# Kernel optimization log

Hardware: AMD Instinct MI355X
Metric: run time of the kernel (lower is better)

## Reference

```python
import jax, jax.numpy as jnp
import numpy as np

B, H, W, DIM = 8, 64, 64, 768
NH = 12
HD = DIM // NH            # 64
WS = 14                   # window size
N = WS * WS               # 196 tokens per window
MLP = 4 * DIM             # 3072
EPS = 1e-5


def layernorm(x, w, b):
    mu = jnp.mean(x, axis=-1, keepdims=True)
    var = jnp.var(x, axis=-1, keepdims=True)
    return (x - mu) * jax.lax.rsqrt(var + EPS) * w + b


def window_partition(x, ws):
    b, h, w, c = x.shape
    pad_h = (ws - h % ws) % ws
    pad_w = (ws - w % ws) % ws
    x = jnp.pad(x, ((0, 0), (0, pad_h), (0, pad_w), (0, 0)))
    hp, wp = h + pad_h, w + pad_w
    x = x.reshape(b, hp // ws, ws, wp // ws, ws, c)
    windows = x.transpose(0, 1, 3, 2, 4, 5).reshape(-1, ws, ws, c)
    return windows, (hp, wp)


def window_unpartition(windows, ws, pad_hw, hw):
    hp, wp = pad_hw
    h, w = hw
    b = windows.shape[0] // (hp * wp // ws // ws)
    x = windows.reshape(b, hp // ws, wp // ws, ws, ws, -1)
    x = x.transpose(0, 1, 3, 2, 4, 5).reshape(b, hp, wp, -1)
    return x[:, :h, :w, :]


def setup_inputs() -> dict:
    key = jax.random.key(0)
    ks = jax.random.split(key, 8)
    f = lambda k, shape: jax.random.normal(k, shape, jnp.float32) * 0.02
    return {
        "x": jax.random.normal(ks[0], (B, H, W, DIM), jnp.float32),
        "n1_w": jnp.ones((DIM,), jnp.float32),
        "n1_b": jnp.zeros((DIM,), jnp.float32),
        "qkv_w": f(ks[1], (DIM, 3 * DIM)),
        "qkv_b": jnp.zeros((3 * DIM,), jnp.float32),
        "proj_w": f(ks[2], (DIM, DIM)),
        "proj_b": jnp.zeros((DIM,), jnp.float32),
        "rel_pos_h": f(ks[3], (2 * WS - 1, HD)),
        "rel_pos_w": f(ks[4], (2 * WS - 1, HD)),
        "n2_w": jnp.ones((DIM,), jnp.float32),
        "n2_b": jnp.zeros((DIM,), jnp.float32),
        "lin1_w": f(ks[5], (DIM, MLP)),
        "lin1_b": jnp.zeros((MLP,), jnp.float32),
        "lin2_w": f(ks[6], (MLP, DIM)),
        "lin2_b": jnp.zeros((DIM,), jnp.float32),
    }


def reference(x, n1_w, n1_b, qkv_w, qkv_b, proj_w, proj_b, rel_pos_h, rel_pos_w,
              n2_w, n2_b, lin1_w, lin1_b, lin2_w, lin2_b):
    shortcut = x
    h = layernorm(x, n1_w, n1_b)
    win, pad_hw = window_partition(h, WS)           # [Bw, WS, WS, DIM]
    bw = win.shape[0]
    qkv = win.reshape(bw, N, DIM) @ qkv_w + qkv_b   # [Bw, N, 3*DIM]
    qkv = qkv.reshape(bw, N, 3, NH, HD).transpose(2, 0, 3, 1, 4)
    qkv = qkv.reshape(3, bw * NH, N, HD)
    q, k, v = qkv[0], qkv[1], qkv[2]
    scale = HD ** -0.5
    attn = jnp.einsum('bqc,bkc->bqk', q * scale, k)  # [Bw*NH, N, N]
    # decomposed rel-pos bias; q_size == k_size == WS so no interpolation
    coords = jnp.arange(WS)[:, None] - jnp.arange(WS)[None, :] + (WS - 1)
    Rh = rel_pos_h[coords]                           # [WS, WS, HD]
    Rw = rel_pos_w[coords]
    r_q = q.reshape(-1, WS, WS, HD)
    rel_h = jnp.einsum('bhwc,hkc->bhwk', r_q, Rh)
    rel_w = jnp.einsum('bhwc,wkc->bhwk', r_q, Rw)
    attn = (attn.reshape(-1, WS, WS, WS, WS)
            + rel_h[:, :, :, :, None]
            + rel_w[:, :, :, None, :]).reshape(-1, N, N)
    attn = jax.nn.softmax(attn, axis=-1)
    out = jnp.einsum('bqk,bkc->bqc', attn, v)        # [Bw*NH, N, HD]
    out = out.reshape(bw, NH, WS, WS, HD).transpose(0, 2, 3, 1, 4)
    out = out.reshape(bw, WS, WS, DIM) @ proj_w + proj_b
    out = window_unpartition(out, WS, pad_hw, (H, W))
    x = shortcut + out
    h2 = layernorm(x, n2_w, n2_b)
    mlp = jax.nn.gelu(h2 @ lin1_w + lin1_b, approximate=False) @ lin2_w + lin2_b
    return x + mlp
```

## Files before the change

### kernel.cpp

```cpp
#include <hip/hip_runtime.h>
#include <hip/hip_bf16.h>
#include <stdint.h>

typedef __attribute__((ext_vector_type(8))) short bf16x8;
typedef __attribute__((ext_vector_type(4))) float f32x4;

__device__ __forceinline__ float bf2f(unsigned short u){
  union { unsigned int i; float f; } v; v.i = ((unsigned int)u) << 16; return v.f;
}
__device__ __forceinline__ unsigned short f2bf(float f){
  union { float f; unsigned int i; } v; v.f = f;
  return (unsigned short)((v.i + 0x7FFFu + ((v.i >> 16) & 1u)) >> 16);
}

__device__ __forceinline__ void gload16(const void* g, void* l){
  __builtin_amdgcn_global_load_lds(
      (const __attribute__((address_space(1))) void*)g,
      (__attribute__((address_space(3))) void*)l, 16, 0, 0);
}

#define VT_OFF 0L
#define Q_OFF  30720000L
#define K_OFF  60825600L

__global__ __launch_bounds__(256) void k_castT(const float* __restrict__ W,
                                               unsigned short* __restrict__ Wt,
                                               int K, int N){
  __shared__ float tl[32][33];
  int ntn = N >> 5;
  int kt = blockIdx.x / ntn, nt = blockIdx.x % ntn;
  int r = threadIdx.x >> 5, c = threadIdx.x & 31;
#pragma unroll
  for (int rr = 0; rr < 4; rr++){
    int row = (kt << 5) + r + (rr << 3);
    tl[r + (rr << 3)][c] = W[(long)row * N + (nt << 5) + c];
  }
  __syncthreads();
#pragma unroll
  for (int rr = 0; rr < 4; rr++){
    int n = (nt << 5) + r + (rr << 3);
    int k = (kt << 5) + c;
    Wt[(long)n * K + k] = f2bf(tl[c][r + (rr << 3)]);
  }
}

__global__ __launch_bounds__(256) void k_ln(const float* __restrict__ X,
                                            const float* __restrict__ w,
                                            const float* __restrict__ b,
                                            unsigned short* __restrict__ out,
                                            int mode){
  int p = blockIdx.x, t = threadIdx.x;
  unsigned short* orow = out + (long)p * 768;
  const float* xrow;
  if (mode == 1){
    int win = p / 196, tok = p - win * 196;
    int bb = win / 25, wrem = win - bb * 25;
    int wy = wrem / 5, wx = wrem - wy * 5;
    int ty = tok / 14, tx = tok - ty * 14;
    int yy = wy * 14 + ty, xx = wx * 14 + tx;
    if (yy >= 64 || xx >= 64){
      for (int j = t; j < 768; j += 256) orow[j] = 0;
      return;
    }
    xrow = X + (long)((bb * 64 + yy) * 64 + xx) * 768;
  } else {
    xrow = X + (long)p * 768;
  }
  float v0 = xrow[t], v1 = xrow[t + 256], v2 = xrow[t + 512];
  float s = v0 + v1 + v2, q = v0 * v0 + v1 * v1 + v2 * v2;
#pragma unroll
  for (int off = 32; off; off >>= 1){ s += __shfl_down(s, off); q += __shfl_down(q, off); }
  __shared__ float ps[4], pq[4], mv[2];
  int wid = t >> 6;
  if ((t & 63) == 0){ ps[wid] = s; pq[wid] = q; }
  __syncthreads();
  if (t == 0){
    float S = ps[0] + ps[1] + ps[2] + ps[3];
    float Q = pq[0] + pq[1] + pq[2] + pq[3];
    float mu = S * (1.0f / 768.0f);
    float var = Q * (1.0f / 768.0f) - mu * mu;
    mv[0] = mu; mv[1] = rsqrtf(var + 1e-5f);
  }
  __syncthreads();
  float mu = mv[0], rs = mv[1];
  orow[t]       = f2bf((v0 - mu) * rs * w[t]       + b[t]);
  orow[t + 256] = f2bf((v1 - mu) * rs * w[t + 256] + b[t + 256]);
  orow[t + 512] = f2bf((v2 - mu) * rs * w[t + 512] + b[t + 512]);
}

template<int MODE>
__global__ __launch_bounds__(256) void k_gemm(const unsigned short* __restrict__ A,
                                              const unsigned short* __restrict__ Bt,
                                              const float* bias,
                                              unsigned short* obf,
                                              float* of32,
                                              const float* addsrc,
                                              int M, int N, int K, int lda, int ldb,
                                              int tilesN){
  __shared__ __align__(16) unsigned short lA[2 * 128 * 32];
  __shared__ __align__(16) unsigned short lB[2 * 128 * 32];
  int t = threadIdx.x;

  int nwg = gridDim.x, bid = blockIdx.x;
  int qq = nwg >> 3, rr = nwg & 7;
  int xcd = bid & 7, oo = bid >> 3;
  int wg = (xcd < rr ? xcd * (qq + 1) : rr * (qq + 1) + (xcd - rr) * qq) + oo;
  int tm = wg / tilesN, tn = wg % tilesN;

  int sl = (t & 3) ^ ((t >> 3) & 3);
  const unsigned short* ga[2]; const unsigned short* gb[2];
#pragma unroll
  for (int c2 = 0; c2 < 2; c2++){
    int i = tm * 128 + c2 * 64 + (t >> 2); if (i > M - 1) i = M - 1;
    ga[c2] = A + (long)i * lda + sl * 8;
    int n = tn * 128 + c2 * 64 + (t >> 2);
    gb[c2] = Bt + (long)n * ldb + sl * 8;
  }

  int lm = t & 15, lg = (t & 63) >> 4, wv = t >> 6;
  int wr = wv >> 1, wc = wv & 1;
  int laneoff = lm * 32 + ((lg ^ ((lm >> 1) & 3)) * 8);

  f32x4 acc[4][4];
#pragma unroll
  for (int a1 = 0; a1 < 4; a1++)
#pragma unroll
    for (int b1 = 0; b1 < 4; b1++) acc[a1][b1] = (f32x4){0.f, 0.f, 0.f, 0.f};

  const int nt = K >> 5;
  {
    unsigned short* la = lA + t * 8;
    unsigned short* lb = lB + t * 8;
    gload16(ga[0], la);
    gload16(ga[1], la + 2048);
    gload16(gb[0], lb);
    gload16(gb[1], lb + 2048);
  }

  for (int tt = 0; tt < nt; tt++){
    int cur = tt & 1;
    if (tt + 1 < nt){
      int k0 = (tt + 1) << 5;
      unsigned short* la = lA + (cur ^ 1) * 4096 + t * 8;
      unsigned short* lb = lB + (cur ^ 1) * 4096 + t * 8;
      gload16(ga[0] + k0, la);
      gload16(ga[1] + k0, la + 2048);
      gload16(gb[0] + k0, lb);
      gload16(gb[1] + k0, lb + 2048);
      asm volatile("s_waitcnt vmcnt(4)" ::: "memory");
    } else {
      asm volatile("s_waitcnt vmcnt(0)" ::: "memory");
    }
    __builtin_amdgcn_sched_barrier(0);
    __builtin_amdgcn_s_barrier();
    __builtin_amdgcn_sched_barrier(0);

    const unsigned short* lap = lA + cur * 4096;
    const unsigned short* lbp = lB + cur * 4096;
    bf16x8 af[4], bfr[4];
#pragma unroll
    for (int mi = 0; mi < 4; mi++)
      af[mi] = *(const bf16x8*)(lap + (wr * 64 + mi * 16) * 32 + laneoff);
#pragma unroll
    for (int ni = 0; ni < 4; ni++)
      bfr[ni] = *(const bf16x8*)(lbp + (wc * 64 + ni * 16) * 32 + laneoff);
    __builtin_amdgcn_s_setprio(1);
#pragma unroll
    for (int mi = 0; mi < 4; mi++)
#pragma unroll
      for (int ni = 0; ni < 4; ni++)
        acc[mi][ni] = __builtin_amdgcn_mfma_f32_16x16x32_bf16(af[mi], bfr[ni], acc[mi][ni], 0, 0, 0);
    __builtin_amdgcn_s_setprio(0);
    __builtin_amdgcn_sched_barrier(0);
    __builtin_amdgcn_s_barrier();
  }

  int i0 = tm * 128 + wr * 64, j0 = tn * 128 + wc * 64;
#pragma unroll
  for (int mi = 0; mi < 4; mi++){
#pragma unroll
    for (int ni = 0; ni < 4; ni++){
      int jc = j0 + ni * 16 + lm;
      float bv = bias ? bias[jc] : 0.0f;
#pragma unroll
      for (int r = 0; r < 4; r++){
        int ir = i0 + mi * 16 + lg * 4 + r;
        float v = acc[mi][ni][r] + bv;
        if (MODE == 0){
          if (ir < M){
            int which = jc / 768, jj = jc - which * 768;
            int head = jj >> 6, cc = jj & 63;
            int win = ir / 196, tok = ir - win * 196;
            long wh = win * 12 + head;
            if (which == 0)      obf[Q_OFF + (wh * 196 + tok) * 64 + cc] = f2bf(v);
            else if (which == 1) obf[K_OFF + (wh * 196 + tok) * 64 + cc] = f2bf(v);
            else                 obf[VT_OFF + (wh * 64 + cc) * 200 + tok] = f2bf(v);
          }
        } else if (MODE == 1){
          if (ir < M){
            int win = ir / 196, tok = ir - win * 196;
            int bb = win / 25, wrem = win - bb * 25;
            int wy = wrem / 5, wx = wrem - wy * 5;
            int yy = wy * 14 + tok / 14, xx = wx * 14 + tok % 14;
            if (yy < 64 && xx < 64){
              long row = (long)((bb * 64 + yy) * 64 + xx);
              of32[row * 768 + jc] = v + addsrc[row * 768 + jc];
            }
          }
        } else if (MODE == 2){
          float g = 0.5f * v * (1.0f + erff(v * 0.70710678118654752f));
          obf[(long)ir * N + jc] = f2bf(g);
        } else {
          long idx = (long)ir * N + jc;
          of32[idx] = v + addsrc[idx];
        }
      }
    }
  }
}

#define KSW(r,c)  ((r) * 64 + ((c) ^ (((r) & 7) << 3)))
#define PSW(q,k)  ((q) * 32 + ((k) ^ (((q) & 3) << 3)))
#define DYN_ATTN  53760
__global__ __launch_bounds__(256, 2) void k_attn(const unsigned short* __restrict__ qb,
                                                 const unsigned short* __restrict__ kb,
                                                 const unsigned short* __restrict__ vtb,
                                                 const float* __restrict__ rph,
                                                 const float* __restrict__ rpw,
                                                 unsigned short* __restrict__ out){
  extern __shared__ __align__(16) char dynsm[];
  unsigned short* Ks = (unsigned short*)dynsm;
  unsigned short* Vt = (unsigned short*)(dynsm + 25088);
  __shared__ __align__(16) unsigned short Pscr[4][2][16 * 32];
  __shared__ unsigned short relhb[2744], relwb[2744];

  int t = threadIdx.x;
  int wh = blockIdx.x;
  int win = wh / 12, head = wh - win * 12;
  const unsigned short* qg  = qb  + (long)wh * 196 * 64;
  const unsigned short* kg  = kb  + (long)wh * 196 * 64;
  const unsigned short* vtg = vtb + (long)wh * 64 * 200;

  int lane = t & 63, wv = t >> 6;
  int lm = lane & 15, lg = lane >> 4;

  for (int ch = t; ch < 1568; ch += 256){
    int row = ch >> 3, c16 = ch & 7;
    gload16(kg + row * 64 + ((c16 ^ (row & 7)) << 3), (char*)Ks + ch * 16);
  }
  {
    int4 zero4 = {0, 0, 0, 0};
    for (int ch = t; ch < 1792; ch += 256){
      int row = ch / 28, c16 = ch - row * 28;
      if (c16 < 25) gload16(vtg + row * 200 + c16 * 8, (char*)Vt + ch * 16);
      else          *(int4*)((char*)Vt + ch * 16) = zero4;
    }
  }

  for (int ty = wv; ty < 14; ty += 4){
    {
      int qa = ty * 14 + lm; if (qa > 195) qa = 195;
      bf16x8 a0 = *(const bf16x8*)(&qg[qa * 64 + lg * 8]);
      bf16x8 a1 = *(const bf16x8*)(&qg[qa * 64 + 32 + lg * 8]);
      int ri = ty - lm + 13; ri = ri < 0 ? 0 : (ri > 26 ? 26 : ri);
      const float* bp = rph + ri * 64 + lg * 8;
      float4 c0 = *(const float4*)(bp),      c1 = *(const float4*)(bp + 4);
      float4 c2 = *(const float4*)(bp + 32), c3 = *(const float4*)(bp + 36);
      bf16x8 b0 = {(short)f2bf(c0.x),(short)f2bf(c0.y),(short)f2bf(c0.z),(short)f2bf(c0.w),
                   (short)f2bf(c1.x),(short)f2bf(c1.y),(short)f2bf(c1.z),(short)f2bf(c1.w)};
      bf16x8 b1 = {(short)f2bf(c2.x),(short)f2bf(c2.y),(short)f2bf(c2.z),(short)f2bf(c2.w),
                   (short)f2bf(c3.x),(short)f2bf(c3.y),(short)f2bf(c3.z),(short)f2bf(c3.w)};
      f32x4 d = (f32x4){0.f, 0.f, 0.f, 0.f};
      d = __builtin_amdgcn_mfma_f32_16x16x32_bf16(a0, b0, d, 0, 0, 0);
      d = __builtin_amdgcn_mfma_f32_16x16x32_bf16(a1, b1, d, 0, 0, 0);
#pragma unroll
      for (int r = 0; r < 4; r++){
        int txr = lg * 4 + r;
        if (txr < 14 && lm < 14) relhb[(ty * 14 + txr) * 14 + lm] = f2bf(d[r]);
      }
    }
    {
      int qa = lm * 14 + ty; if (qa > 195) qa = 195;
      bf16x8 a0 = *(const bf16x8*)(&qg[qa * 64 + lg * 8]);
      bf16x8 a1 = *(const bf16x8*)(&qg[qa * 64 + 32 + lg * 8]);
      int ri = ty - lm + 13; ri = ri < 0 ? 0 : (ri > 26 ? 26 : ri);
      const float* bp = rpw + ri * 64 + lg * 8;
      float4 c0 = *(const float4*)(bp),      c1 = *(const float4*)(bp + 4);
      float4 c2 = *(const float4*)(bp + 32), c3 = *(const float4*)(bp + 36);
      bf16x8 b0 = {(short)f2bf(c0.x),(short)f2bf(c0.y),(short)f2bf(c0.z),(short)f2bf(c0.w),
                   (short)f2bf(c1.x),(short)f2bf(c1.y),(short)f2bf(c1.z),(short)f2bf(c1.w)};
      bf16x8 b1 = {(short)f2bf(c2.x),(short)f2bf(c2.y),(short)f2bf(c2.z),(short)f2bf(c2.w),
                   (short)f2bf(c3.x),(short)f2bf(c3.y),(short)f2bf(c3.z),(short)f2bf(c3.w)};
      f32x4 d = (f32x4){0.f, 0.f, 0.f, 0.f};
      d = __builtin_amdgcn_mfma_f32_16x16x32_bf16(a0, b0, d, 0, 0, 0);
      d = __builtin_amdgcn_mfma_f32_16x16x32_bf16(a1, b1, d, 0, 0, 0);
#pragma unroll
      for (int r = 0; r < 4; r++){
        int tyr = lg * 4 + r;
        if (tyr < 14 && lm < 14) relwb[(tyr * 14 + ty) * 14 + lm] = f2bf(d[r]);
      }
    }
  }
  __syncthreads();

  int khw[13];
#pragma unroll
  for (int nt = 0; nt < 13; nt++){
    int kc = nt * 16 + lm;
    khw[nt] = (kc < 196) ? (((kc / 14) << 4) | (kc % 14)) : -1;
  }

  for (int mt = wv; mt < 13; mt += 4){
    int qr = mt * 16 + lm; if (qr > 195) qr = 195;
    bf16x8 aq0 = *(const bf16x8*)(&qg[qr * 64 + lg * 8]);
    bf16x8 aq1 = *(const bf16x8*)(&qg[qr * 64 + 32 + lg * 8]);
    f32x4 sacc[13];
#pragma unroll
    for (int nt = 0; nt < 13; nt++) sacc[nt] = (f32x4){0.f, 0.f, 0.f, 0.f};
#pragma unroll
    for (int nt = 0; nt < 13; nt++){
      int kr = nt * 16 + lm; if (kr > 195) kr = 195;
      bf16x8 bk0 = *(const bf16x8*)(&Ks[KSW(kr, lg * 8)]);
      bf16x8 bk1 = *(const bf16x8*)(&Ks[KSW(kr, 32 + lg * 8)]);
      sacc[nt] = __builtin_amdgcn_mfma_f32_16x16x32_bf16(aq0, bk0, sacc[nt], 0, 0, 0);
      sacc[nt] = __builtin_amdgcn_mfma_f32_16x16x32_bf16(aq1, bk1, sacc[nt], 0, 0, 0);
    }
    float rinv[4];
#pragma unroll
    for (int r = 0; r < 4; r++){
      int qrow = mt * 16 + lg * 4 + r;
      int qb14 = (qrow < 196) ? qrow * 14 : 0;
      float mx = -1e30f;
#pragma unroll
      for (int nt = 0; nt < 13; nt++){
        float s;
        if (khw[nt] >= 0)
          s = sacc[nt][r] * 0.125f + bf2f(relhb[qb14 + (khw[nt] >> 4)])
                                   + bf2f(relwb[qb14 + (khw[nt] & 15)]);
        else s = -1e30f;
        sacc[nt][r] = s; mx = fmaxf(mx, s);
      }
      mx = fmaxf(mx, __shfl_xor(mx, 1));
      mx = fmaxf(mx, __shfl_xor(mx, 2));
      mx = fmaxf(mx, __shfl_xor(mx, 4));
      mx = fmaxf(mx, __shfl_xor(mx, 8));
      float sum = 0.f;
#pragma unroll
      for (int nt = 0; nt < 13; nt++){
        float p = __expf(sacc[nt][r] - mx);
        sum += p;
        sacc[nt][r] = p;
      }
      sum += __shfl_xor(sum, 1); sum += __shfl_xor(sum, 2);
      sum += __shfl_xor(sum, 4); sum += __shfl_xor(sum, 8);
      rinv[r] = 1.0f / sum;
    }
    f32x4 oacc[4];
#pragma unroll
    for (int vt = 0; vt < 4; vt++) oacc[vt] = (f32x4){0.f, 0.f, 0.f, 0.f};
#pragma unroll
    for (int kk = 0; kk < 7; kk++){
      unsigned short* Ps = &Pscr[wv][kk & 1][0];
      int nt0 = 2 * kk, nt1 = 2 * kk + 1;
#pragma unroll
      for (int r = 0; r < 4; r++){
        int q = lg * 4 + r;
        Ps[PSW(q, lm)]      = f2bf(sacc[nt0][r]);
        Ps[PSW(q, lm + 16)] = (nt1 < 13) ? f2bf(sacc[nt1][r]) : (unsigned short)0;
      }
      bf16x8 ap = *(const bf16x8*)(&Ps[PSW(lm, lg * 8)]);
#pragma unroll
      for (int vt = 0; vt < 4; vt++){
        bf16x8 bv = *(const bf16x8*)(&Vt[(vt * 16 + lm) * 224 + kk * 32 + lg * 8]);
        oacc[vt] = __builtin_amdgcn_mfma_f32_16x16x32_bf16(ap, bv, oacc[vt], 0, 0, 0);
      }
    }
#pragma unroll
    for (int vt = 0; vt < 4; vt++){
#pragma unroll
      for (int r = 0; r < 4; r++){
        int orow = mt * 16 + lg * 4 + r;
        if (orow < 196)
          out[(long)(win * 196 + orow) * 768 + head * 64 + vt * 16 + lm] =
              f2bf(oacc[vt][r] * rinv[r]);
      }
    }
  }
}

static const long O_W     = 60211200;
static const long O_PROJT = 63750144;
static const long O_L1T   = 64929792;
static const long O_L2T   = 69648384;
static const long O_R2    = 74366976;
static const unsigned long WS_FULL = 275693568UL;

extern "C" void kernel_launch(void* const* d_in, const int* in_sizes, int n_in,
                              void* d_out, int out_size, void* d_ws, size_t ws_size,
                              hipStream_t stream){
  const float* x     = (const float*)d_in[0];
  const float* n1w   = (const float*)d_in[1];
  const float* n1b   = (const float*)d_in[2];
  const float* qkvw  = (const float*)d_in[3];
  const float* qkvb  = (const float*)d_in[4];
  const float* projw = (const float*)d_in[5];
  const float* projb = (const float*)d_in[6];
  const float* rph   = (const float*)d_in[7];
  const float* rpw   = (const float*)d_in[8];
  const float* n2w   = (const float*)d_in[9];
  const float* n2b   = (const float*)d_in[10];
  const float* l1w   = (const float*)d_in[11];
  const float* l1b   = (const float*)d_in[12];
  const float* l2w   = (const float*)d_in[13];
  const float* l2b   = (const float*)d_in[14];
  float* out = (float*)d_out;
  char* ws = (char*)d_ws;

  unsigned short* hpad   = (unsigned short*)(ws);
  unsigned short* attout = (unsigned short*)(ws);
  unsigned short* h2     = (unsigned short*)(ws);
  unsigned short* wqkvT  = (unsigned short*)(ws + O_W);
  unsigned short* wprojT = (unsigned short*)(ws + O_PROJT);
  unsigned short* wl1T   = (unsigned short*)(ws + O_L1T);
  unsigned short* wl2T   = (unsigned short*)(ws + O_L2T);
  unsigned short* r2     = (unsigned short*)(ws + O_R2);
  unsigned short* hidden = (unsigned short*)(ws + O_R2);

  const unsigned short* vtbuf = r2 + VT_OFF;
  const unsigned short* qbuf  = r2 + Q_OFF;
  const unsigned short* kbuf  = r2 + K_OFF;

  const bool full = (ws_size >= WS_FULL);

  k_castT<<<(768 / 32) * (2304 / 32), 256, 0, stream>>>(qkvw, wqkvT, 768, 2304);
  k_castT<<<(768 / 32) * (768 / 32),  256, 0, stream>>>(projw, wprojT, 768, 768);
  k_castT<<<(768 / 32) * (3072 / 32), 256, 0, stream>>>(l1w, wl1T, 768, 3072);
  k_castT<<<(3072 / 32) * (768 / 32), 256, 0, stream>>>(l2w, wl2T, 3072, 768);

  k_ln<<<39200, 256, 0, stream>>>(x, n1w, n1b, hpad, 1);

  k_gemm<0><<<307 * 18, 256, 0, stream>>>(hpad, wqkvT, qkvb, r2, nullptr, nullptr,
                                          39200, 2304, 768, 768, 768, 18);

  (void)hipFuncSetAttribute((const void*)k_attn,
                            hipFuncAttributeMaxDynamicSharedMemorySize, DYN_ATTN);
  k_attn<<<2400, 256, DYN_ATTN, stream>>>(qbuf, kbuf, vtbuf, rph, rpw, attout);

  k_gemm<1><<<307 * 6, 256, 0, stream>>>(attout, wprojT, projb, nullptr, out, x,
                                         39200, 768, 768, 768, 768, 6);

  k_ln<<<32768, 256, 0, stream>>>(out, n2w, n2b, h2, 0);

  if (full){
    k_gemm<2><<<256 * 24, 256, 0, stream>>>(h2, wl1T, l1b, hidden, nullptr, nullptr,
                                            32768, 3072, 768, 768, 768, 24);
    k_gemm<3><<<256 * 6, 256, 0, stream>>>(hidden, wl2T, l2b, nullptr, out, out,
                                           32768, 768, 3072, 3072, 3072, 6);
  } else {
    for (int c = 0; c < 2; c++){
      k_gemm<2><<<256 * 12, 256, 0, stream>>>(h2, wl1T + (long)c * 1536 * 768,
                                              l1b + c * 1536, hidden, nullptr, nullptr,
                                              32768, 1536, 768, 768, 768, 12);
      k_gemm<3><<<256 * 6, 256, 0, stream>>>(hidden, wl2T + c * 1536,
                                             c == 0 ? l2b : nullptr, nullptr, out, out,
                                             32768, 768, 1536, 1536, 3072, 6);
    }
  }
}
```

Measured before the change: 1.312 ms.

## Enlarge GEMM tiles to 256x256x64 with 512 threads and dynamic LDS

Rewrites the shared GEMM kernel to use 256x256 output tiles with a K-step of 64, 8 waves per block, and 128 KB of dynamically allocated double-buffered LDS. It also uses an XOR swizzle on 16-byte chunks and splits each K-step into four MFMA phases separated by barriers. The goal is higher arithmetic intensity per LDS and global load, fewer blocks, and less redundant traffic across all four linear layers. In exchange it limits occupancy to one block per CU, uses far more accumulator registers, and leaves fewer tiles for load balancing, especially on the M=39200 GEMMs with partial last tiles.

```diff
diff --git a/kernel.cpp b/kernel.cpp
--- a/kernel.cpp
+++ b/kernel.cpp
@@ -88,17 +88,19 @@
   orow[t + 512] = f2bf((v2 - mu) * rs * w[t + 512] + b[t + 512]);
 }
 
+#define GEMM_LDS 131072
 template<int MODE>
-__global__ __launch_bounds__(256) void k_gemm(const unsigned short* __restrict__ A,
-                                              const unsigned short* __restrict__ Bt,
-                                              const float* bias,
-                                              unsigned short* obf,
-                                              float* of32,
-                                              const float* addsrc,
-                                              int M, int N, int K, int lda, int ldb,
-                                              int tilesN){
-  __shared__ __align__(16) unsigned short lA[2 * 128 * 32];
-  __shared__ __align__(16) unsigned short lB[2 * 128 * 32];
+__global__ __launch_bounds__(512, 1) void k_gemm(const unsigned short* __restrict__ A,
+                                                 const unsigned short* __restrict__ Bt,
+                                                 const float* bias,
+                                                 unsigned short* obf,
+                                                 float* of32,
+                                                 const float* addsrc,
+                                                 int M, int N, int K, int lda, int ldb,
+                                                 int tilesN){
+  extern __shared__ __align__(16) char gsm[];
+  unsigned short* lAb = (unsigned short*)gsm;
+  unsigned short* lBb = (unsigned short*)(gsm + 65536);
   int t = threadIdx.x;
 
   int nwg = gridDim.x, bid = blockIdx.x;
@@ -107,47 +109,53 @@
   int wg = (xcd < rr ? xcd * (qq + 1) : rr * (qq + 1) + (xcd - rr) * qq) + oo;
   int tm = wg / tilesN, tn = wg % tilesN;
 
-  int sl = (t & 3) ^ ((t >> 3) & 3);
-  const unsigned short* ga[2]; const unsigned short* gb[2];
-#pragma unroll
-  for (int c2 = 0; c2 < 2; c2++){
-    int i = tm * 128 + c2 * 64 + (t >> 2); if (i > M - 1) i = M - 1;
-    ga[c2] = A + (long)i * lda + sl * 8;
-    int n = tn * 128 + c2 * 64 + (t >> 2);
-    gb[c2] = Bt + (long)n * ldb + sl * 8;
-  }
-
-  int lm = t & 15, lg = (t & 63) >> 4, wv = t >> 6;
-  int wr = wv >> 1, wc = wv & 1;
-  int laneoff = lm * 32 + ((lg ^ ((lm >> 1) & 3)) * 8);
-
-  f32x4 acc[4][4];
-#pragma unroll
-  for (int a1 = 0; a1 < 4; a1++)
-#pragma unroll
-    for (int b1 = 0; b1 < 4; b1++) acc[a1][b1] = (f32x4){0.f, 0.f, 0.f, 0.f};
-
-  const int nt = K >> 5;
-  {
-    unsigned short* la = lA + t * 8;
-    unsigned short* lb = lB + t * 8;
-    gload16(ga[0], la);
-    gload16(ga[1], la + 2048);
-    gload16(gb[0], lb);
-    gload16(gb[1], lb + 2048);
+  const unsigned short* gA[4]; const unsigned short* gB[4];
+#pragma unroll
+  for (int c = 0; c < 4; c++){
+    int ch = t + c * 512;
+    int row = ch >> 3, c16 = ch & 7;
+    int ia = tm * 256 + row; if (ia > M - 1) ia = M - 1;
+    gA[c] = A + (long)ia * lda + ((c16 ^ (row & 7)) << 3);
+    int nb = tn * 256 + row;
+    gB[c] = Bt + (long)nb * ldb + ((c16 ^ (row & 7)) << 3);
+  }
+
+  int lane = t & 63, wid = t >> 6;
+  int wm = wid >> 2, wn = wid & 3;
+  int lm = lane & 15, lg = lane >> 4;
+  int sw = (lm & 7) << 3;
+  int arow = (wm * 128 + lm) * 64;
+  int brow = (wn * 64 + lm) * 64;
+  int col0 = (lg * 8) ^ sw;
+  int col1 = (32 + lg * 8) ^ sw;
+
+  f32x4 acc[8][4];
+#pragma unroll
+  for (int mi = 0; mi < 8; mi++)
+#pragma unroll
+    for (int ni = 0; ni < 4; ni++) acc[mi][ni] = (f32x4){0.f, 0.f, 0.f, 0.f};
+
+  const int nt = K >> 6;
+#pragma unroll
+  for (int c = 0; c < 4; c++){
+    int ch = t + c * 512;
+    gload16(gA[c], (char*)lAb + ch * 16);
+    gload16(gB[c], (char*)lBb + ch * 16);
   }
 
   for (int tt = 0; tt < nt; tt++){
     int cur = tt & 1;
     if (tt + 1 < nt){
-      int k0 = (tt + 1) << 5;
-      unsigned short* la = lA + (cur ^ 1) * 4096 + t * 8;
-      unsigned short* lb = lB + (cur ^ 1) * 4096 + t * 8;
-      gload16(ga[0] + k0, la);
-      gload16(ga[1] + k0, la + 2048);
-      gload16(gb[0] + k0, lb);
-      gload16(gb[1] + k0, lb + 2048);
-      asm volatile("s_waitcnt vmcnt(4)" ::: "memory");
+      long k0 = (long)(tt + 1) << 6;
+      char* la = (char*)(lAb + (cur ^ 1) * 16384);
+      char* lb = (char*)(lBb + (cur ^ 1) * 16384);
+#pragma unroll
+      for (int c = 0; c < 4; c++){
+        int ch = t + c * 512;
+        gload16(gA[c] + k0, la + ch * 16);
+        gload16(gB[c] + k0, lb + ch * 16);
+      }
+      asm volatile("s_waitcnt vmcnt(8)" ::: "memory");
     } else {
       asm volatile("s_waitcnt vmcnt(0)" ::: "memory");
     }
@@ -155,29 +163,70 @@
     __builtin_amdgcn_s_barrier();
     __builtin_amdgcn_sched_barrier(0);
 
-    const unsigned short* lap = lA + cur * 4096;
-    const unsigned short* lbp = lB + cur * 4096;
-    bf16x8 af[4], bfr[4];
+    const unsigned short* la = lAb + cur * 16384;
+    const unsigned short* lb = lBb + cur * 16384;
+
+    bf16x8 bk[4], af[4];
+#pragma unroll
+    for (int ni = 0; ni < 4; ni++) bk[ni] = *(const bf16x8*)(lb + brow + ni * 1024 + col0);
+#pragma unroll
+    for (int mi = 0; mi < 4; mi++) af[mi] = *(const bf16x8*)(la + arow + mi * 1024 + col0);
+    __builtin_amdgcn_s_setprio(1);
 #pragma unroll
     for (int mi = 0; mi < 4; mi++)
-      af[mi] = *(const bf16x8*)(lap + (wr * 64 + mi * 16) * 32 + laneoff);
-#pragma unroll
-    for (int ni = 0; ni < 4; ni++)
-      bfr[ni] = *(const bf16x8*)(lbp + (wc * 64 + ni * 16) * 32 + laneoff);
+#pragma unroll
+      for (int ni = 0; ni < 4; ni++)
+        acc[mi][ni] = __builtin_amdgcn_mfma_f32_16x16x32_bf16(af[mi], bk[ni], acc[mi][ni], 0, 0, 0);
+    __builtin_amdgcn_s_setprio(0);
+    __builtin_amdgcn_sched_barrier(0);
+    __builtin_amdgcn_s_barrier();
+    __builtin_amdgcn_sched_barrier(0);
+
+#pragma unroll
+    for (int mi = 0; mi < 4; mi++) af[mi] = *(const bf16x8*)(la + arow + (mi + 4) * 1024 + col0);
     __builtin_amdgcn_s_setprio(1);
 #pragma unroll
     for (int mi = 0; mi < 4; mi++)
 #pragma unroll
       for (int ni = 0; ni < 4; ni++)
-        acc[mi][ni] = __builtin_amdgcn_mfma_f32_16x16x32_bf16(af[mi], bfr[ni], acc[mi][ni], 0, 0, 0);
+        acc[mi + 4][ni] = __builtin_amdgcn_mfma_f32_16x16x32_bf16(af[mi], bk[ni], acc[mi + 4][ni], 0, 0, 0);
     __builtin_amdgcn_s_setprio(0);
     __builtin_amdgcn_sched_barrier(0);
     __builtin_amdgcn_s_barrier();
-  }
-
-  int i0 = tm * 128 + wr * 64, j0 = tn * 128 + wc * 64;
-#pragma unroll
-  for (int mi = 0; mi < 4; mi++){
+    __builtin_amdgcn_sched_barrier(0);
+
+#pragma unroll
+    for (int ni = 0; ni < 4; ni++) bk[ni] = *(const bf16x8*)(lb + brow + ni * 1024 + col1);
+#pragma unroll
+    for (int mi = 0; mi < 4; mi++) af[mi] = *(const bf16x8*)(la + arow + mi * 1024 + col1);
+    __builtin_amdgcn_s_setprio(1);
+#pragma unroll
+    for (int mi = 0; mi < 4; mi++)
+#pragma unroll
+      for (int ni = 0; ni < 4; ni++)
+        acc[mi][ni] = __builtin_amdgcn_mfma_f32_16x16x32_bf16(af[mi], bk[ni], acc[mi][ni], 0, 0, 0);
+    __builtin_amdgcn_s_setprio(0);
+    __builtin_amdgcn_sched_barrier(0);
+    __builtin_amdgcn_s_barrier();
+    __builtin_amdgcn_sched_barrier(0);
+
+#pragma unroll
+    for (int mi = 0; mi < 4; mi++) af[mi] = *(const bf16x8*)(la + arow + (mi + 4) * 1024 + col1);
+    __builtin_amdgcn_s_setprio(1);
+#pragma unroll
+    for (int mi = 0; mi < 4; mi++)
+#pragma unroll
+      for (int ni = 0; ni < 4; ni++)
+        acc[mi + 4][ni] = __builtin_amdgcn_mfma_f32_16x16x32_bf16(af[mi], bk[ni], acc[mi + 4][ni], 0, 0, 0);
+    __builtin_amdgcn_s_setprio(0);
+    __builtin_amdgcn_sched_barrier(0);
+    __builtin_amdgcn_s_barrier();
+    __builtin_amdgcn_sched_barrier(0);
+  }
+
+  int i0 = tm * 256 + wm * 128, j0 = tn * 256 + wn * 64;
+#pragma unroll
+  for (int mi = 0; mi < 8; mi++){
 #pragma unroll
     for (int ni = 0; ni < 4; ni++){
       int jc = j0 + ni * 16 + lm;
@@ -432,6 +481,17 @@
 
   const bool full = (ws_size >= WS_FULL);
 
+  (void)hipFuncSetAttribute(reinterpret_cast<const void*>(&k_gemm<0>),
+                            hipFuncAttributeMaxDynamicSharedMemorySize, GEMM_LDS);
+  (void)hipFuncSetAttribute(reinterpret_cast<const void*>(&k_gemm<1>),
+                            hipFuncAttributeMaxDynamicSharedMemorySize, GEMM_LDS);
+  (void)hipFuncSetAttribute(reinterpret_cast<const void*>(&k_gemm<2>),
+                            hipFuncAttributeMaxDynamicSharedMemorySize, GEMM_LDS);
+  (void)hipFuncSetAttribute(reinterpret_cast<const void*>(&k_gemm<3>),
+                            hipFuncAttributeMaxDynamicSharedMemorySize, GEMM_LDS);
+  (void)hipFuncSetAttribute(reinterpret_cast<const void*>(&k_attn),
+                            hipFuncAttributeMaxDynamicSharedMemorySize, DYN_ATTN);
+
   k_castT<<<(768 / 32) * (2304 / 32), 256, 0, stream>>>(qkvw, wqkvT, 768, 2304);
   k_castT<<<(768 / 32) * (768 / 32),  256, 0, stream>>>(projw, wprojT, 768, 768);
   k_castT<<<(768 / 32) * (3072 / 32), 256, 0, stream>>>(l1w, wl1T, 768, 3072);
@@ -439,31 +499,29 @@
 
   k_ln<<<39200, 256, 0, stream>>>(x, n1w, n1b, hpad, 1);
 
-  k_gemm<0><<<307 * 18, 256, 0, stream>>>(hpad, wqkvT, qkvb, r2, nullptr, nullptr,
-                                          39200, 2304, 768, 768, 768, 18);
-
-  (void)hipFuncSetAttribute((const void*)k_attn,
-                            hipFuncAttributeMaxDynamicSharedMemorySize, DYN_ATTN);
+  k_gemm<0><<<154 * 9, 512, GEMM_LDS, stream>>>(hpad, wqkvT, qkvb, r2, nullptr, nullptr,
+                                                39200, 2304, 768, 768, 768, 9);
+
   k_attn<<<2400, 256, DYN_ATTN, stream>>>(qbuf, kbuf, vtbuf, rph, rpw, attout);
 
-  k_gemm<1><<<307 * 6, 256, 0, stream>>>(attout, wprojT, projb, nullptr, out, x,
-                                         39200, 768, 768, 768, 768, 6);
+  k_gemm<1><<<154 * 3, 512, GEMM_LDS, stream>>>(attout, wprojT, projb, nullptr, out, x,
+                                                39200, 768, 768, 768, 768, 3);
 
   k_ln<<<32768, 256, 0, stream>>>(out, n2w, n2b, h2, 0);
 
   if (full){
-    k_gemm<2><<<256 * 24, 256, 0, stream>>>(h2, wl1T, l1b, hidden, nullptr, nullptr,
-                                            32768, 3072, 768, 768, 768, 24);
-    k_gemm<3><<<256 * 6, 256, 0, stream>>>(hidden, wl2T, l2b, nullptr, out, out,
-                                           32768, 768, 3072, 3072, 3072, 6);
+    k_gemm<2><<<128 * 12, 512, GEMM_LDS, stream>>>(h2, wl1T, l1b, hidden, nullptr, nullptr,
+                                                   32768, 3072, 768, 768, 768, 12);
+    k_gemm<3><<<128 * 3, 512, GEMM_LDS, stream>>>(hidden, wl2T, l2b, nullptr, out, out,
+                                                  32768, 768, 3072, 3072, 3072, 3);
   } else {
     for (int c = 0; c < 2; c++){
-      k_gemm<2><<<256 * 12, 256, 0, stream>>>(h2, wl1T + (long)c * 1536 * 768,
-                                              l1b + c * 1536, hidden, nullptr, nullptr,
-                                              32768, 1536, 768, 768, 768, 12);
-      k_gemm<3><<<256 * 6, 256, 0, stream>>>(hidden, wl2T + c * 1536,
-                                             c == 0 ? l2b : nullptr, nullptr, out, out,
-                                             32768, 768, 1536, 1536, 3072, 6);
-    }
-  }
-}
+      k_gemm<2><<<128 * 6, 512, GEMM_LDS, stream>>>(h2, wl1T + (long)c * 1536 * 768,
+                                                    l1b + c * 1536, hidden, nullptr, nullptr,
+                                                    32768, 1536, 768, 768, 768, 6);
+      k_gemm<3><<<128 * 3, 512, GEMM_LDS, stream>>>(hidden, wl2T + c * 1536,
+                                                    c == 0 ? l2b : nullptr, nullptr, out, out,
+                                                    32768, 768, 1536, 1536, 3072, 3);
+    }
+  }
+}
```

New measurement: 1.490 ms. 13.5% more time.

## Enlarge GEMM M-tile to 256 rows with 128x64 per-wave subtiles

Applied to the files above, without the earlier changes.

The GEMM kernel's block tile grows from 128x128 to 256x128. Each wave now computes a 128x64 output with 8x4 MFMA accumulators and reuses each B fragment across two halves of A. The aim is to raise arithmetic intensity and cut global and LDS traffic per FLOP. Costs are more accumulator registers, doubled A LDS space, fewer workgroups (which may hurt occupancy and load balance) and more padding waste on M=39200. The attention smem attribute call is also moved earlier.

```diff
diff --git a/kernel.cpp b/kernel.cpp
--- a/kernel.cpp
+++ b/kernel.cpp
@@ -97,7 +97,7 @@
                                               const float* addsrc,
                                               int M, int N, int K, int lda, int ldb,
                                               int tilesN){
-  __shared__ __align__(16) unsigned short lA[2 * 128 * 32];
+  __shared__ __align__(16) unsigned short lA[2 * 256 * 32];
   __shared__ __align__(16) unsigned short lB[2 * 128 * 32];
   int t = threadIdx.x;
 
@@ -107,47 +107,54 @@
   int wg = (xcd < rr ? xcd * (qq + 1) : rr * (qq + 1) + (xcd - rr) * qq) + oo;
   int tm = wg / tilesN, tn = wg % tilesN;
 
-  int sl = (t & 3) ^ ((t >> 3) & 3);
-  const unsigned short* ga[2]; const unsigned short* gb[2];
-#pragma unroll
-  for (int c2 = 0; c2 < 2; c2++){
-    int i = tm * 128 + c2 * 64 + (t >> 2); if (i > M - 1) i = M - 1;
-    ga[c2] = A + (long)i * lda + sl * 8;
-    int n = tn * 128 + c2 * 64 + (t >> 2);
-    gb[c2] = Bt + (long)n * ldb + sl * 8;
-  }
-
-  int lm = t & 15, lg = (t & 63) >> 4, wv = t >> 6;
-  int wr = wv >> 1, wc = wv & 1;
-  int laneoff = lm * 32 + ((lg ^ ((lm >> 1) & 3)) * 8);
-
-  f32x4 acc[4][4];
-#pragma unroll
-  for (int a1 = 0; a1 < 4; a1++)
-#pragma unroll
-    for (int b1 = 0; b1 < 4; b1++) acc[a1][b1] = (f32x4){0.f, 0.f, 0.f, 0.f};
+  const unsigned short* gA[4]; const unsigned short* gB[2];
+#pragma unroll
+  for (int c = 0; c < 4; c++){
+    int ch = t + c * 256;
+    int row = ch >> 2, c16 = ch & 3;
+    int ia = tm * 256 + row; if (ia > M - 1) ia = M - 1;
+    gA[c] = A + (long)ia * lda + ((c16 ^ ((row >> 1) & 3)) << 3);
+  }
+#pragma unroll
+  for (int c = 0; c < 2; c++){
+    int ch = t + c * 256;
+    int row = ch >> 2, c16 = ch & 3;
+    int nb = tn * 128 + row;
+    gB[c] = Bt + (long)nb * ldb + ((c16 ^ ((row >> 1) & 3)) << 3);
+  }
+
+  int lane = t & 63, wv = t >> 6;
+  int wm = wv >> 1, wn = wv & 1;
+  int lm = lane & 15, lg = lane >> 4;
+  int colk = (lg ^ ((lm >> 1) & 3)) * 8;
+  int abase = (wm * 128 + lm) * 32 + colk;
+  int bbase = (wn * 64 + lm) * 32 + colk;
+
+  f32x4 acc[8][4];
+#pragma unroll
+  for (int mi = 0; mi < 8; mi++)
+#pragma unroll
+    for (int ni = 0; ni < 4; ni++) acc[mi][ni] = (f32x4){0.f, 0.f, 0.f, 0.f};
 
   const int nt = K >> 5;
   {
-    unsigned short* la = lA + t * 8;
-    unsigned short* lb = lB + t * 8;
-    gload16(ga[0], la);
-    gload16(ga[1], la + 2048);
-    gload16(gb[0], lb);
-    gload16(gb[1], lb + 2048);
+#pragma unroll
+    for (int c = 0; c < 4; c++) gload16(gA[c], (char*)lA + (t + c * 256) * 16);
+#pragma unroll
+    for (int c = 0; c < 2; c++) gload16(gB[c], (char*)lB + (t + c * 256) * 16);
   }
 
   for (int tt = 0; tt < nt; tt++){
     int cur = tt & 1;
     if (tt + 1 < nt){
-      int k0 = (tt + 1) << 5;
-      unsigned short* la = lA + (cur ^ 1) * 4096 + t * 8;
-      unsigned short* lb = lB + (cur ^ 1) * 4096 + t * 8;
-      gload16(ga[0] + k0, la);
-      gload16(ga[1] + k0, la + 2048);
-      gload16(gb[0] + k0, lb);
-      gload16(gb[1] + k0, lb + 2048);
-      asm volatile("s_waitcnt vmcnt(4)" ::: "memory");
+      long k0 = (long)(tt + 1) << 5;
+      char* la = (char*)(lA + (cur ^ 1) * 8192);
+      char* lb = (char*)(lB + (cur ^ 1) * 4096);
+#pragma unroll
+      for (int c = 0; c < 4; c++) gload16(gA[c] + k0, la + (t + c * 256) * 16);
+#pragma unroll
+      for (int c = 0; c < 2; c++) gload16(gB[c] + k0, lb + (t + c * 256) * 16);
+      asm volatile("s_waitcnt vmcnt(6)" ::: "memory");
     } else {
       asm volatile("s_waitcnt vmcnt(0)" ::: "memory");
     }
@@ -155,29 +162,33 @@
     __builtin_amdgcn_s_barrier();
     __builtin_amdgcn_sched_barrier(0);
 
-    const unsigned short* lap = lA + cur * 4096;
-    const unsigned short* lbp = lB + cur * 4096;
-    bf16x8 af[4], bfr[4];
-#pragma unroll
-    for (int mi = 0; mi < 4; mi++)
-      af[mi] = *(const bf16x8*)(lap + (wr * 64 + mi * 16) * 32 + laneoff);
-#pragma unroll
-    for (int ni = 0; ni < 4; ni++)
-      bfr[ni] = *(const bf16x8*)(lbp + (wc * 64 + ni * 16) * 32 + laneoff);
-    __builtin_amdgcn_s_setprio(1);
-#pragma unroll
-    for (int mi = 0; mi < 4; mi++)
-#pragma unroll
-      for (int ni = 0; ni < 4; ni++)
-        acc[mi][ni] = __builtin_amdgcn_mfma_f32_16x16x32_bf16(af[mi], bfr[ni], acc[mi][ni], 0, 0, 0);
-    __builtin_amdgcn_s_setprio(0);
+    const unsigned short* la = lA + cur * 8192;
+    const unsigned short* lb = lB + cur * 4096;
+    bf16x8 bk[4];
+#pragma unroll
+    for (int ni = 0; ni < 4; ni++) bk[ni] = *(const bf16x8*)(lb + bbase + ni * 512);
+#pragma unroll
+    for (int half = 0; half < 2; half++){
+      bf16x8 af[4];
+#pragma unroll
+      for (int mi = 0; mi < 4; mi++)
+        af[mi] = *(const bf16x8*)(la + abase + (half * 4 + mi) * 512);
+      __builtin_amdgcn_s_setprio(1);
+#pragma unroll
+      for (int mi = 0; mi < 4; mi++)
+#pragma unroll
+        for (int ni = 0; ni < 4; ni++)
+          acc[half * 4 + mi][ni] =
+              __builtin_amdgcn_mfma_f32_16x16x32_bf16(af[mi], bk[ni], acc[half * 4 + mi][ni], 0, 0, 0);
+      __builtin_amdgcn_s_setprio(0);
+    }
     __builtin_amdgcn_sched_barrier(0);
     __builtin_amdgcn_s_barrier();
   }
 
-  int i0 = tm * 128 + wr * 64, j0 = tn * 128 + wc * 64;
-#pragma unroll
-  for (int mi = 0; mi < 4; mi++){
+  int i0 = tm * 256 + wm * 128, j0 = tn * 128 + wn * 64;
+#pragma unroll
+  for (int mi = 0; mi < 8; mi++){
 #pragma unroll
     for (int ni = 0; ni < 4; ni++){
       int jc = j0 + ni * 16 + lm;
@@ -432,6 +443,9 @@
 
   const bool full = (ws_size >= WS_FULL);
 
+  (void)hipFuncSetAttribute(reinterpret_cast<const void*>(&k_attn),
+                            hipFuncAttributeMaxDynamicSharedMemorySize, DYN_ATTN);
+
   k_castT<<<(768 / 32) * (2304 / 32), 256, 0, stream>>>(qkvw, wqkvT, 768, 2304);
   k_castT<<<(768 / 32) * (768 / 32),  256, 0, stream>>>(projw, wprojT, 768, 768);
   k_castT<<<(768 / 32) * (3072 / 32), 256, 0, stream>>>(l1w, wl1T, 768, 3072);
@@ -439,29 +453,27 @@
 
   k_ln<<<39200, 256, 0, stream>>>(x, n1w, n1b, hpad, 1);
 
-  k_gemm<0><<<307 * 18, 256, 0, stream>>>(hpad, wqkvT, qkvb, r2, nullptr, nullptr,
+  k_gemm<0><<<154 * 18, 256, 0, stream>>>(hpad, wqkvT, qkvb, r2, nullptr, nullptr,
                                           39200, 2304, 768, 768, 768, 18);
 
-  (void)hipFuncSetAttribute((const void*)k_attn,
-                            hipFuncAttributeMaxDynamicSharedMemorySize, DYN_ATTN);
   k_attn<<<2400, 256, DYN_ATTN, stream>>>(qbuf, kbuf, vtbuf, rph, rpw, attout);
 
-  k_gemm<1><<<307 * 6, 256, 0, stream>>>(attout, wprojT, projb, nullptr, out, x,
+  k_gemm<1><<<154 * 6, 256, 0, stream>>>(attout, wprojT, projb, nullptr, out, x,
                                          39200, 768, 768, 768, 768, 6);
 
   k_ln<<<32768, 256, 0, stream>>>(out, n2w, n2b, h2, 0);
 
   if (full){
-    k_gemm<2><<<256 * 24, 256, 0, stream>>>(h2, wl1T, l1b, hidden, nullptr, nullptr,
+    k_gemm<2><<<128 * 24, 256, 0, stream>>>(h2, wl1T, l1b, hidden, nullptr, nullptr,
                                             32768, 3072, 768, 768, 768, 24);
-    k_gemm<3><<<256 * 6, 256, 0, stream>>>(hidden, wl2T, l2b, nullptr, out, out,
+    k_gemm<3><<<128 * 6, 256, 0, stream>>>(hidden, wl2T, l2b, nullptr, out, out,
                                            32768, 768, 3072, 3072, 3072, 6);
   } else {
     for (int c = 0; c < 2; c++){
-      k_gemm<2><<<256 * 12, 256, 0, stream>>>(h2, wl1T + (long)c * 1536 * 768,
+      k_gemm<2><<<128 * 12, 256, 0, stream>>>(h2, wl1T + (long)c * 1536 * 768,
                                               l1b + c * 1536, hidden, nullptr, nullptr,
                                               32768, 1536, 768, 768, 768, 12);
-      k_gemm<3><<<256 * 6, 256, 0, stream>>>(hidden, wl2T + c * 1536,
+      k_gemm<3><<<128 * 6, 256, 0, stream>>>(hidden, wl2T + c * 1536,
                                              c == 0 ? l2b : nullptr, nullptr, out, out,
                                              32768, 768, 1536, 1536, 3072, 6);
     }
```

Measured after the change: 2.231 ms. +70.0%, slower.
